# Optimization experiments

Hardware: AMD Instinct MI355X
Metric: run time of the kernel (lower is better)

The kernel has to match this reference:

```python
import jax, jax.numpy as jnp
import numpy as np

N_LEVELS = 16
F_PER_LEVEL = 2
LOG2_T = 19
TABLE_SIZE = 1 << LOG2_T
BASE_RES = 16.0
FINEST_RES = 512.0
# W == H == 512 -> x1 = y1 = 1.0
BOX_MIN = jnp.array([-1.0, -1.0], dtype=jnp.float32)
BOX_MAX = jnp.array([1.0, 1.0], dtype=jnp.float32)
# corner offsets, same order as torch BOX_OFFSETS: (0,0),(0,1),(1,0),(1,1)
OFFSETS = jnp.array([[i, j] for i in (0, 1) for j in (0, 1)], dtype=jnp.int32)
PRIME0 = jnp.uint32(1)
PRIME1 = jnp.uint32(2654435761)
HASH_MASK = jnp.uint32(TABLE_SIZE - 1)


def setup_inputs() -> dict:
    key = jax.random.key(0)
    ks = jax.random.split(key, 8)
    B, P = 4, 262144
    coord_2D = jax.random.uniform(ks[0], (B, P, 2), dtype=jnp.float32)  # in [0,1) subset of box
    embeddings = jax.random.normal(ks[1], (N_LEVELS, TABLE_SIZE, F_PER_LEVEL), dtype=jnp.float32)
    d_in = 2 + N_LEVELS * F_PER_LEVEL  # 34
    W0 = jax.random.normal(ks[2], (d_in, 256), dtype=jnp.float32) * 0.05
    b0 = jnp.zeros((256,), dtype=jnp.float32)
    W1 = jax.random.normal(ks[3], (256, 256), dtype=jnp.float32) * 0.05
    b1 = jnp.zeros((256,), dtype=jnp.float32)
    W2 = jax.random.normal(ks[4], (256, 3), dtype=jnp.float32) * 0.05
    b2 = jnp.zeros((3,), dtype=jnp.float32)
    return {"coord_2D": coord_2D, "embeddings": embeddings,
            "W0": W0, "b0": b0, "W1": W1, "b1": b1, "W2": W2, "b2": b2}


def _hash(corners_int32):
    # corners: [N,4,2] int32; xor of per-dim prime products, masked to table size (uint32 wraparound semantics)
    c = corners_int32.astype(jnp.uint32)
    h = (c[..., 0] * PRIME0) ^ (c[..., 1] * PRIME1)
    return (h & HASH_MASK).astype(jnp.int32)


def _encode(xy, embeddings):
    # xy: [N,2]; embeddings: [L, T, F]
    b = np.exp((np.log(FINEST_RES) - np.log(BASE_RES)) / (N_LEVELS - 1))
    resolutions = jnp.floor(BASE_RES * (b ** jnp.arange(N_LEVELS, dtype=jnp.float32)))  # [L]

    def level_encode(table, res):
        grid = (BOX_MAX - BOX_MIN) / res                     # [2]
        bl = jnp.floor((xy - BOX_MIN) / grid).astype(jnp.int32)  # bottom-left cell idx [N,2]
        vmin = bl.astype(xy.dtype) * grid + BOX_MIN          # voxel min vertex [N,2]
        w = (xy - vmin) / grid                               # bilinear weights [N,2]
        corners = bl[:, None, :] + OFFSETS                   # [N,4,2]
        emb = table[_hash(corners)]                          # gather: [N,4,F]
        wx = w[:, 0:1]
        wy = w[:, 1:2]
        c00 = emb[:, 0] * (1 - wx) + emb[:, 2] * wx
        c01 = emb[:, 1] * (1 - wx) + emb[:, 3] * wx
        return c00 * (1 - wy) + c01 * wy                     # [N,F]

    enc = jax.vmap(level_encode)(embeddings, resolutions)    # [L,N,F]
    return jnp.moveaxis(enc, 0, 1).reshape(xy.shape[0], N_LEVELS * F_PER_LEVEL)


def reference(coord_2D, embeddings, W0, b0, W1, b1, W2, b2):
    B = coord_2D.shape[0]
    xy = jnp.clip(coord_2D.reshape(-1, 2), BOX_MIN, BOX_MAX)
    enc = _encode(xy, embeddings)
    points_enc = jnp.concatenate([xy, enc], axis=-1)         # [N, 34]
    feat = jax.nn.relu(points_enc @ W0 + b0)
    feat = jax.nn.relu(feat @ W1 + b1)
    rgb = jax.nn.sigmoid(feat @ W2 + b2)
    return rgb.reshape(B, -1, 3)
```

## Files before the change

kernel.cpp:

```cpp
#include <hip/hip_runtime.h>
#include <hip/hip_bf16.h>
#include <cstdint>
#include <cstddef>

#define N_LEVELS   16
#define LOG2_T     19
#define TABLE_SIZE (1u << LOG2_T)
#define HASH_MASK  (TABLE_SIZE - 1u)
#define PRIME1     2654435761u

#define TPB 256
#define BT  64

typedef __attribute__((ext_vector_type(8))) short short8;
typedef __attribute__((ext_vector_type(4))) float floatx4;
typedef __attribute__((ext_vector_type(2))) float f32x2;

__device__ __forceinline__ constexpr float resf(int l) {
    constexpr float r[N_LEVELS] = {
        16.f, 20.f, 25.f, 32.f, 40.f, 50.f, 64.f, 80.f,
        101.f, 128.f, 161.f, 203.f, 256.f, 322.f, 406.f, 512.f
    };
    return r[l];
}

__device__ __forceinline__ unsigned short f2bf(float x) {
    union { float f; uint32_t u; } v; v.f = x;
    const uint32_t u = v.u;
    return (unsigned short)((u + 0x7fffu + ((u >> 16) & 1u)) >> 16);
}

__device__ __forceinline__ uint32_t pk_bf16(float a, float b) {
#if __has_builtin(__builtin_amdgcn_cvt_pk_bf16_f32)
    typedef __attribute__((ext_vector_type(2))) __bf16 bf16x2;
    bf16x2 v = __builtin_amdgcn_cvt_pk_bf16_f32(a, b);
    uint32_t u; __builtin_memcpy(&u, &v, 4); return u;
#else
    return (uint32_t)f2bf(a) | ((uint32_t)f2bf(b) << 16);
#endif
}

__device__ __forceinline__ int fswz(int row, int cb) {
    return (row << 7) + (cb ^ ((row & 7) << 4));
}
__device__ __forceinline__ int hswz(int row, int cb) {
    const int c = row & 7;
    return (row << 9) + (cb ^ ((c << 4) ^ (c << 6)));
}

__global__ void pack_weights(const float* __restrict__ W0,
                             const float* __restrict__ W1,
                             const float* __restrict__ W2,
                             unsigned short* __restrict__ ws)
{
    const int f = blockIdx.x;
    const int lane = threadIdx.x;
    const int q = lane >> 4, r = lane & 15;
    int layer, kt, nt;
    if (f < 32)       { layer = 0; kt = f >> 4;        nt = f & 15; }
    else if (f < 160) { layer = 1; kt = (f - 32) >> 4; nt = (f - 32) & 15; }
    else              { layer = 2; kt = f - 160;       nt = 0; }
    unsigned short vals[8];
    #pragma unroll
    for (int j = 0; j < 8; ++j) {
        const int k = kt * 32 + q * 8 + j;
        const int n = nt * 16 + r;
        float v = 0.f;
        if (layer == 0) {
            if (k < 32)       v = W0[(2 + k) * 256 + n];
            else if (k == 32) v = W0[0 * 256 + n];
            else if (k == 33) v = W0[1 * 256 + n];
        } else if (layer == 1) {
            v = W1[k * 256 + n];
        } else {
            if (n < 3) v = W2[k * 3 + n];
        }
        vals[j] = f2bf(v);
    }
    uint4 pk;
    pk.x = (uint32_t)vals[0] | ((uint32_t)vals[1] << 16);
    pk.y = (uint32_t)vals[2] | ((uint32_t)vals[3] << 16);
    pk.z = (uint32_t)vals[4] | ((uint32_t)vals[5] << 16);
    pk.w = (uint32_t)vals[6] | ((uint32_t)vals[7] << 16);
    *(uint4*)(ws + (size_t)f * 1024 + lane * 8) = pk;
}

template<int G>
__device__ __forceinline__ uint4 encode4(float x, float y, const char* __restrict__ ebase)
{
    uint32_t vv[4];
    #pragma unroll
    for (int i = 0; i < 4; ++i) {
        const int l = 4 * G + i;
        const float res  = resf(l);
        const float grid = 2.0f / res;
        const float invg = res * 0.5f;
        const float tx = (x + 1.0f) / grid;
        const float ty = (y + 1.0f) / grid;
        const int bx = (int)floorf(tx);
        const int by = (int)floorf(ty);
        const float wx = (x - ((float)bx * grid - 1.0f)) * invg;
        const float wy = (y - ((float)by * grid - 1.0f)) * invg;
        const uint32_t hy0 = (uint32_t)by * PRIME1;
        const uint32_t hy1 = hy0 + PRIME1;
        const uint32_t ux0 = (uint32_t)bx;
        const uint32_t ux1 = ux0 + 1u;
        const uint32_t lb = (uint32_t)l << (LOG2_T + 3);
        const f32x2 e00 = *(const f32x2*)(ebase + (lb + (((ux0 ^ hy0) & HASH_MASK) << 3)));
        const f32x2 e01 = *(const f32x2*)(ebase + (lb + (((ux0 ^ hy1) & HASH_MASK) << 3)));
        const f32x2 e10 = *(const f32x2*)(ebase + (lb + (((ux1 ^ hy0) & HASH_MASK) << 3)));
        const f32x2 e11 = *(const f32x2*)(ebase + (lb + (((ux1 ^ hy1) & HASH_MASK) << 3)));
        const float owx = 1.f - wx, owy = 1.f - wy;
        const float f0 = (e00.x * owx + e10.x * wx) * owy + (e01.x * owx + e11.x * wx) * wy;
        const float f1 = (e00.y * owx + e10.y * wx) * owy + (e01.y * owx + e11.y * wx) * wy;
        vv[i] = pk_bf16(f0, f1);
    }
    uint4 v; v.x = vv[0]; v.y = vv[1]; v.z = vv[2]; v.w = vv[3];
    return v;
}

__device__ __forceinline__ uint2 bias_relu_pk(const floatx4 a, const float4 bias)
{
    const f32x2 z = {0.f, 0.f};
    f32x2 v01 = {a[0], a[1]};
    f32x2 v23 = {a[2], a[3]};
    const f32x2 b01 = {bias.x, bias.y};
    const f32x2 b23 = {bias.z, bias.w};
    v01 += b01;
    v23 += b23;
    v01 = __builtin_elementwise_max(v01, z);
    v23 = __builtin_elementwise_max(v23, z);
    uint2 r;
    r.x = pk_bf16(v01.x, v01.y);
    r.y = pk_bf16(v23.x, v23.y);
    return r;
}

__global__ __launch_bounds__(TPB, 4)
void fused_ngp_mlp(const float2* __restrict__ xy,
                   const float* __restrict__ emb,
                   const unsigned short* __restrict__ wpack,
                   const float* __restrict__ b0,
                   const float* __restrict__ b1,
                   const float* __restrict__ b2,
                   float* __restrict__ out, int npoints)
{
    __shared__ __attribute__((aligned(16))) unsigned char feat[BT * 128];
    __shared__ __attribute__((aligned(16))) unsigned char h[BT * 512];

    const int t = threadIdx.x;
    const int p0 = blockIdx.x * BT;
    const int wave = t >> 6;
    const int lane = t & 63;
    const int q = lane >> 4, r = lane & 15;

    {
        const int p = t >> 2;
        const int sg = t & 3;
        const int gp = p0 + p;
        float x = 0.f, y = 0.f;
        if (gp < npoints) {
            const float2 c = xy[gp];
            x = fminf(fmaxf(c.x, -1.f), 1.f);
            y = fminf(fmaxf(c.y, -1.f), 1.f);
        }
        uint4 z = {0u, 0u, 0u, 0u};
        if (sg == 0) z.x = pk_bf16(x, y);
        *(uint4*)(feat + fswz(p, 64 + 16 * sg)) = z;
    }

    {
        const int p = lane;
        const int gp = p0 + p;
        float x = 0.f, y = 0.f;
        if (gp < npoints) {
            const float2 c = xy[gp];
            x = fminf(fmaxf(c.x, -1.f), 1.f);
            y = fminf(fmaxf(c.y, -1.f), 1.f);
        }
        const char* ebase = (const char*)emb;
        uint4 v;
        switch (wave) {
            case 0:  v = encode4<0>(x, y, ebase); break;
            case 1:  v = encode4<1>(x, y, ebase); break;
            case 2:  v = encode4<2>(x, y, ebase); break;
            default: v = encode4<3>(x, y, ebase); break;
        }
        *(uint4*)(feat + fswz(p, 16 * wave)) = v;
    }
    __syncthreads();

    const unsigned short* w0p = wpack;
    const unsigned short* w1p = wpack + 32 * 1024;
    const unsigned short* w2p = wpack + 160 * 1024;

    {
        floatx4 acc[4][4];
        #pragma unroll
        for (int mti = 0; mti < 4; ++mti)
            #pragma unroll
            for (int nt = 0; nt < 4; ++nt)
                acc[mti][nt] = floatx4{0.f, 0.f, 0.f, 0.f};
        #pragma unroll
        for (int kt = 0; kt < 2; ++kt) {
            short8 a[4], b[4];
            #pragma unroll
            for (int mti = 0; mti < 4; ++mti)
                a[mti] = *(const short8*)(w0p + (size_t)(kt * 16 + wave * 4 + mti) * 1024 + lane * 8);
            #pragma unroll
            for (int nt = 0; nt < 4; ++nt)
                b[nt] = *(const short8*)(feat + fswz(16 * nt + r, 64 * kt + 16 * q));
            #pragma unroll
            for (int mti = 0; mti < 4; ++mti)
                #pragma unroll
                for (int nt = 0; nt < 4; ++nt)
                    acc[mti][nt] = __builtin_amdgcn_mfma_f32_16x16x32_bf16(a[mti], b[nt], acc[mti][nt], 0, 0, 0);
        }
        #pragma unroll
        for (int mti = 0; mti < 4; ++mti) {
            const int col = (wave * 4 + mti) * 16 + 4 * q;
            const float4 bias = *(const float4*)&b0[col];
            #pragma unroll
            for (int nt = 0; nt < 4; ++nt) {
                const uint2 v = bias_relu_pk(acc[mti][nt], bias);
                *(uint2*)(h + hswz(16 * nt + r, 2 * col)) = v;
            }
        }
    }
    __syncthreads();

    {
        floatx4 acc[4][4];
        #pragma unroll
        for (int mti = 0; mti < 4; ++mti)
            #pragma unroll
            for (int nt = 0; nt < 4; ++nt)
                acc[mti][nt] = floatx4{0.f, 0.f, 0.f, 0.f};
        #pragma unroll 2
        for (int kt = 0; kt < 8; ++kt) {
            short8 a[4], b[4];
            #pragma unroll
            for (int mti = 0; mti < 4; ++mti)
                a[mti] = *(const short8*)(w1p + (size_t)(kt * 16 + wave * 4 + mti) * 1024 + lane * 8);
            #pragma unroll
            for (int nt = 0; nt < 4; ++nt)
                b[nt] = *(const short8*)(h + hswz(16 * nt + r, 64 * kt + 16 * q));
            #pragma unroll
            for (int mti = 0; mti < 4; ++mti)
                #pragma unroll
                for (int nt = 0; nt < 4; ++nt)
                    acc[mti][nt] = __builtin_amdgcn_mfma_f32_16x16x32_bf16(a[mti], b[nt], acc[mti][nt], 0, 0, 0);
        }
        __syncthreads();
        #pragma unroll
        for (int mti = 0; mti < 4; ++mti) {
            const int col = (wave * 4 + mti) * 16 + 4 * q;
            const float4 bias = *(const float4*)&b1[col];
            #pragma unroll
            for (int nt = 0; nt < 4; ++nt) {
                const uint2 v = bias_relu_pk(acc[mti][nt], bias);
                *(uint2*)(h + hswz(16 * nt + r, 2 * col)) = v;
            }
        }
    }
    __syncthreads();

    {
        floatx4 acc = floatx4{0.f, 0.f, 0.f, 0.f};
        #pragma unroll
        for (int kt = 0; kt < 8; ++kt) {
            const short8 a = *(const short8*)(w2p + (size_t)kt * 1024 + lane * 8);
            const short8 b = *(const short8*)(h + hswz(16 * wave + r, 64 * kt + 16 * q));
            acc = __builtin_amdgcn_mfma_f32_16x16x32_bf16(a, b, acc, 0, 0, 0);
        }
        if (q == 0) {
            const int gp = p0 + 16 * wave + r;
            if (gp < npoints) {
                #pragma unroll
                for (int reg = 0; reg < 3; ++reg) {
                    const float s = acc[reg] + b2[reg];
                    out[(size_t)gp * 3 + reg] = 1.f / (1.f + expf(-s));
                }
            }
        }
    }
}

extern "C" void kernel_launch(void* const* d_in, const int* in_sizes, int n_in,
                              void* d_out, int out_size, void* d_ws, size_t ws_size,
                              hipStream_t stream) {
    const float* coord = (const float*)d_in[0];
    const float* emb   = (const float*)d_in[1];
    const float* W0    = (const float*)d_in[2];
    const float* b0    = (const float*)d_in[3];
    const float* W1    = (const float*)d_in[4];
    const float* b1    = (const float*)d_in[5];
    const float* W2    = (const float*)d_in[6];
    const float* b2    = (const float*)d_in[7];
    float* out = (float*)d_out;
    unsigned short* ws = (unsigned short*)d_ws;

    const int npoints = in_sizes[0] / 2;
    const int blocks  = (npoints + BT - 1) / BT;

    hipLaunchKernelGGL(pack_weights, dim3(168), dim3(64), 0, stream, W0, W1, W2, ws);
    hipLaunchKernelGGL(fused_ngp_mlp, dim3(blocks), dim3(TPB), 0, stream,
                       (const float2*)coord, emb, ws, b0, b1, b2, out, npoints);
}
```

Measured before the change: 355.1 us.

## Use 512-thread blocks: 8 waves split hash levels and MLP N tiles

Doubles the block to 8 waves. Each wave now encodes 2 hash levels instead of 4, and the MLP tiles are split so each wave computes 4 M tiles by 2 point tiles. The separate feat LDS buffer is aliased onto h, with an extra barrier before layer-0 results overwrite it, which cuts LDS per block. The aim is more waves in flight to hide gather latency and lower per-thread register pressure, at the cost of loading each weight fragment from global twice per block and adding synchronisation.

```diff
diff --git a/kernel.cpp b/kernel.cpp
--- a/kernel.cpp
+++ b/kernel.cpp
@@ -9,7 +9,7 @@
 #define HASH_MASK  (TABLE_SIZE - 1u)
 #define PRIME1     2654435761u
 
-#define TPB 256
+#define TPB 512
 #define BT  64
 
 typedef __attribute__((ext_vector_type(8))) short short8;
@@ -85,13 +85,13 @@
     *(uint4*)(ws + (size_t)f * 1024 + lane * 8) = pk;
 }
 
-template<int G>
-__device__ __forceinline__ uint4 encode4(float x, float y, const char* __restrict__ ebase)
+template<int W>
+__device__ __forceinline__ uint2 encode2(float x, float y, const char* __restrict__ ebase)
 {
-    uint32_t vv[4];
+    uint32_t vv[2];
     #pragma unroll
-    for (int i = 0; i < 4; ++i) {
-        const int l = 4 * G + i;
+    for (int i = 0; i < 2; ++i) {
+        const int l = 2 * W + i;
         const float res  = resf(l);
         const float grid = 2.0f / res;
         const float invg = res * 0.5f;
@@ -115,7 +115,7 @@
         const float f1 = (e00.y * owx + e10.y * wx) * owy + (e01.y * owx + e11.y * wx) * wy;
         vv[i] = pk_bf16(f0, f1);
     }
-    uint4 v; v.x = vv[0]; v.y = vv[1]; v.z = vv[2]; v.w = vv[3];
+    uint2 v; v.x = vv[0]; v.y = vv[1];
     return v;
 }
 
@@ -136,7 +136,7 @@
     return r;
 }
 
-__global__ __launch_bounds__(TPB, 4)
+__global__ __launch_bounds__(TPB, 6)
 void fused_ngp_mlp(const float2* __restrict__ xy,
                    const float* __restrict__ emb,
                    const unsigned short* __restrict__ wpack,
@@ -145,48 +145,55 @@
                    const float* __restrict__ b2,
                    float* __restrict__ out, int npoints)
 {
-    __shared__ __attribute__((aligned(16))) unsigned char feat[BT * 128];
     __shared__ __attribute__((aligned(16))) unsigned char h[BT * 512];
+    unsigned char* feat = h;
 
     const int t = threadIdx.x;
     const int p0 = blockIdx.x * BT;
     const int wave = t >> 6;
     const int lane = t & 63;
     const int q = lane >> 4, r = lane & 15;
+    const int wn = wave & 3;
+    const int wp = wave >> 2;
 
     {
-        const int p = t >> 2;
-        const int sg = t & 3;
-        const int gp = p0 + p;
+        const int p = t >> 3;
+        const int sg = t & 7;
+        uint2 z = {0u, 0u};
+        if (sg == 0) {
+            const int gp = p0 + p;
+            float x = 0.f, y = 0.f;
+            if (gp < npoints) {
+                const float2 c = xy[gp];
+                x = fminf(fmaxf(c.x, -1.f), 1.f);
+                y = fminf(fmaxf(c.y, -1.f), 1.f);
+            }
+            z.x = pk_bf16(x, y);
+        }
+        *(uint2*)(feat + fswz(p, 64 + 8 * sg)) = z;
+    }
+
+    {
+        const int gp = p0 + lane;
         float x = 0.f, y = 0.f;
         if (gp < npoints) {
             const float2 c = xy[gp];
             x = fminf(fmaxf(c.x, -1.f), 1.f);
             y = fminf(fmaxf(c.y, -1.f), 1.f);
         }
-        uint4 z = {0u, 0u, 0u, 0u};
-        if (sg == 0) z.x = pk_bf16(x, y);
-        *(uint4*)(feat + fswz(p, 64 + 16 * sg)) = z;
-    }
-
-    {
-        const int p = lane;
-        const int gp = p0 + p;
-        float x = 0.f, y = 0.f;
-        if (gp < npoints) {
-            const float2 c = xy[gp];
-            x = fminf(fmaxf(c.x, -1.f), 1.f);
-            y = fminf(fmaxf(c.y, -1.f), 1.f);
-        }
         const char* ebase = (const char*)emb;
-        uint4 v;
+        uint2 v;
         switch (wave) {
-            case 0:  v = encode4<0>(x, y, ebase); break;
-            case 1:  v = encode4<1>(x, y, ebase); break;
-            case 2:  v = encode4<2>(x, y, ebase); break;
-            default: v = encode4<3>(x, y, ebase); break;
-        }
-        *(uint4*)(feat + fswz(p, 16 * wave)) = v;
+            case 0:  v = encode2<0>(x, y, ebase); break;
+            case 1:  v = encode2<1>(x, y, ebase); break;
+            case 2:  v = encode2<2>(x, y, ebase); break;
+            case 3:  v = encode2<3>(x, y, ebase); break;
+            case 4:  v = encode2<4>(x, y, ebase); break;
+            case 5:  v = encode2<5>(x, y, ebase); break;
+            case 6:  v = encode2<6>(x, y, ebase); break;
+            default: v = encode2<7>(x, y, ebase); break;
+        }
+        *(uint2*)(feat + fswz(lane, 8 * wave)) = v;
     }
     __syncthreads();
 
@@ -195,77 +202,76 @@
     const unsigned short* w2p = wpack + 160 * 1024;
 
     {
-        floatx4 acc[4][4];
+        floatx4 acc[4][2];
         #pragma unroll
         for (int mti = 0; mti < 4; ++mti)
             #pragma unroll
-            for (int nt = 0; nt < 4; ++nt)
+            for (int nt = 0; nt < 2; ++nt)
                 acc[mti][nt] = floatx4{0.f, 0.f, 0.f, 0.f};
         #pragma unroll
         for (int kt = 0; kt < 2; ++kt) {
-            short8 a[4], b[4];
-            #pragma unroll
-            for (int mti = 0; mti < 4; ++mti)
-                a[mti] = *(const short8*)(w0p + (size_t)(kt * 16 + wave * 4 + mti) * 1024 + lane * 8);
-            #pragma unroll
-            for (int nt = 0; nt < 4; ++nt)
-                b[nt] = *(const short8*)(feat + fswz(16 * nt + r, 64 * kt + 16 * q));
-            #pragma unroll
-            for (int mti = 0; mti < 4; ++mti)
+            short8 b[2];
+            #pragma unroll
+            for (int nt = 0; nt < 2; ++nt)
+                b[nt] = *(const short8*)(feat + fswz((wp * 2 + nt) * 16 + r, 64 * kt + 16 * q));
+            #pragma unroll
+            for (int mti = 0; mti < 4; ++mti) {
+                const short8 a = *(const short8*)(w0p + (size_t)(kt * 16 + wn * 4 + mti) * 1024 + lane * 8);
                 #pragma unroll
-                for (int nt = 0; nt < 4; ++nt)
-                    acc[mti][nt] = __builtin_amdgcn_mfma_f32_16x16x32_bf16(a[mti], b[nt], acc[mti][nt], 0, 0, 0);
-        }
+                for (int nt = 0; nt < 2; ++nt)
+                    acc[mti][nt] = __builtin_amdgcn_mfma_f32_16x16x32_bf16(a, b[nt], acc[mti][nt], 0, 0, 0);
+            }
+        }
+        __syncthreads();
         #pragma unroll
         for (int mti = 0; mti < 4; ++mti) {
-            const int col = (wave * 4 + mti) * 16 + 4 * q;
+            const int col = (wn * 4 + mti) * 16 + 4 * q;
             const float4 bias = *(const float4*)&b0[col];
             #pragma unroll
-            for (int nt = 0; nt < 4; ++nt) {
+            for (int nt = 0; nt < 2; ++nt) {
                 const uint2 v = bias_relu_pk(acc[mti][nt], bias);
-                *(uint2*)(h + hswz(16 * nt + r, 2 * col)) = v;
+                *(uint2*)(h + hswz((wp * 2 + nt) * 16 + r, 2 * col)) = v;
             }
         }
     }
     __syncthreads();
 
     {
-        floatx4 acc[4][4];
+        floatx4 acc[4][2];
         #pragma unroll
         for (int mti = 0; mti < 4; ++mti)
             #pragma unroll
-            for (int nt = 0; nt < 4; ++nt)
+            for (int nt = 0; nt < 2; ++nt)
                 acc[mti][nt] = floatx4{0.f, 0.f, 0.f, 0.f};
         #pragma unroll 2
         for (int kt = 0; kt < 8; ++kt) {
-            short8 a[4], b[4];
-            #pragma unroll
-            for (int mti = 0; mti < 4; ++mti)
-                a[mti] = *(const short8*)(w1p + (size_t)(kt * 16 + wave * 4 + mti) * 1024 + lane * 8);
-            #pragma unroll
-            for (int nt = 0; nt < 4; ++nt)
-                b[nt] = *(const short8*)(h + hswz(16 * nt + r, 64 * kt + 16 * q));
-            #pragma unroll
-            for (int mti = 0; mti < 4; ++mti)
+            short8 b[2];
+            #pragma unroll
+            for (int nt = 0; nt < 2; ++nt)
+                b[nt] = *(const short8*)(h + hswz((wp * 2 + nt) * 16 + r, 64 * kt + 16 * q));
+            #pragma unroll
+            for (int mti = 0; mti < 4; ++mti) {
+                const short8 a = *(const short8*)(w1p + (size_t)(kt * 16 + wn * 4 + mti) * 1024 + lane * 8);
                 #pragma unroll
-                for (int nt = 0; nt < 4; ++nt)
-                    acc[mti][nt] = __builtin_amdgcn_mfma_f32_16x16x32_bf16(a[mti], b[nt], acc[mti][nt], 0, 0, 0);
+                for (int nt = 0; nt < 2; ++nt)
+                    acc[mti][nt] = __builtin_amdgcn_mfma_f32_16x16x32_bf16(a, b[nt], acc[mti][nt], 0, 0, 0);
+            }
         }
         __syncthreads();
         #pragma unroll
         for (int mti = 0; mti < 4; ++mti) {
-            const int col = (wave * 4 + mti) * 16 + 4 * q;
+            const int col = (wn * 4 + mti) * 16 + 4 * q;
             const float4 bias = *(const float4*)&b1[col];
             #pragma unroll
-            for (int nt = 0; nt < 4; ++nt) {
+            for (int nt = 0; nt < 2; ++nt) {
                 const uint2 v = bias_relu_pk(acc[mti][nt], bias);
-                *(uint2*)(h + hswz(16 * nt + r, 2 * col)) = v;
+                *(uint2*)(h + hswz((wp * 2 + nt) * 16 + r, 2 * col)) = v;
             }
         }
     }
     __syncthreads();
 
-    {
+    if (wave < 4) {
         floatx4 acc = floatx4{0.f, 0.f, 0.f, 0.f};
         #pragma unroll
         for (int kt = 0; kt < 8; ++kt) {
```

New measurement: 428.8 us. 1.21x slower.

## Fold xy rows of W0 into epilogue FMAs and alias feature LDS into hidden buffer

Applied to the files above, without the earlier changes.

The xy contribution to layer 0 is now computed in fp32 with scalar FMAs in the bias/ReLU epilogue, using W0 rows read directly from global memory. This halves the first MFMA K-loop to one 32-wide step over the hash features only. The separate feature shared buffer is removed by aliasing it onto the hidden buffer, with an added barrier before overwriting. The aim is fewer MFMAs and less LDS per block, which may raise occupancy. The cost is extra coordinate loads per thread and more per-element FMAs, and it relies on pack_weights laying out the K rows so that tile 0 holds only the encoding features.

```diff
diff --git a/kernel.cpp b/kernel.cpp
--- a/kernel.cpp
+++ b/kernel.cpp
@@ -140,13 +140,14 @@
 void fused_ngp_mlp(const float2* __restrict__ xy,
                    const float* __restrict__ emb,
                    const unsigned short* __restrict__ wpack,
+                   const float* __restrict__ W0g,
                    const float* __restrict__ b0,
                    const float* __restrict__ b1,
                    const float* __restrict__ b2,
                    float* __restrict__ out, int npoints)
 {
-    __shared__ __attribute__((aligned(16))) unsigned char feat[BT * 128];
     __shared__ __attribute__((aligned(16))) unsigned char h[BT * 512];
+    unsigned char* feat = h;
 
     const int t = threadIdx.x;
     const int p0 = blockIdx.x * BT;
@@ -154,19 +155,15 @@
     const int lane = t & 63;
     const int q = lane >> 4, r = lane & 15;
 
-    {
-        const int p = t >> 2;
-        const int sg = t & 3;
-        const int gp = p0 + p;
-        float x = 0.f, y = 0.f;
-        if (gp < npoints) {
-            const float2 c = xy[gp];
-            x = fminf(fmaxf(c.x, -1.f), 1.f);
-            y = fminf(fmaxf(c.y, -1.f), 1.f);
-        }
-        uint4 z = {0u, 0u, 0u, 0u};
-        if (sg == 0) z.x = pk_bf16(x, y);
-        *(uint4*)(feat + fswz(p, 64 + 16 * sg)) = z;
+    float cx[4], cy[4];
+    #pragma unroll
+    for (int nt = 0; nt < 4; ++nt) {
+        const int gp2 = p0 + 16 * nt + r;
+        float2 c;
+        if (gp2 < npoints) c = xy[gp2];
+        else { c.x = 0.f; c.y = 0.f; }
+        cx[nt] = fminf(fmaxf(c.x, -1.f), 1.f);
+        cy[nt] = fminf(fmaxf(c.y, -1.f), 1.f);
     }
 
     {
@@ -201,28 +198,38 @@
             #pragma unroll
             for (int nt = 0; nt < 4; ++nt)
                 acc[mti][nt] = floatx4{0.f, 0.f, 0.f, 0.f};
-        #pragma unroll
-        for (int kt = 0; kt < 2; ++kt) {
+        {
             short8 a[4], b[4];
             #pragma unroll
             for (int mti = 0; mti < 4; ++mti)
-                a[mti] = *(const short8*)(w0p + (size_t)(kt * 16 + wave * 4 + mti) * 1024 + lane * 8);
+                a[mti] = *(const short8*)(w0p + (size_t)(wave * 4 + mti) * 1024 + lane * 8);
             #pragma unroll
             for (int nt = 0; nt < 4; ++nt)
-                b[nt] = *(const short8*)(feat + fswz(16 * nt + r, 64 * kt + 16 * q));
+                b[nt] = *(const short8*)(feat + fswz(16 * nt + r, 16 * q));
             #pragma unroll
             for (int mti = 0; mti < 4; ++mti)
                 #pragma unroll
                 for (int nt = 0; nt < 4; ++nt)
                     acc[mti][nt] = __builtin_amdgcn_mfma_f32_16x16x32_bf16(a[mti], b[nt], acc[mti][nt], 0, 0, 0);
         }
+        __syncthreads();
         #pragma unroll
         for (int mti = 0; mti < 4; ++mti) {
             const int col = (wave * 4 + mti) * 16 + 4 * q;
             const float4 bias = *(const float4*)&b0[col];
+            const float4 w0x  = *(const float4*)&W0g[col];
+            const float4 w0y  = *(const float4*)&W0g[256 + col];
             #pragma unroll
             for (int nt = 0; nt < 4; ++nt) {
-                const uint2 v = bias_relu_pk(acc[mti][nt], bias);
+                const float x = cx[nt], y = cy[nt];
+                floatx4 aa = acc[mti][nt];
+                aa[0] += bias.x + x * w0x.x + y * w0y.x;
+                aa[1] += bias.y + x * w0x.y + y * w0y.y;
+                aa[2] += bias.z + x * w0x.z + y * w0y.z;
+                aa[3] += bias.w + x * w0x.w + y * w0y.w;
+                uint2 v;
+                v.x = pk_bf16(fmaxf(aa[0], 0.f), fmaxf(aa[1], 0.f));
+                v.y = pk_bf16(fmaxf(aa[2], 0.f), fmaxf(aa[3], 0.f));
                 *(uint2*)(h + hswz(16 * nt + r, 2 * col)) = v;
             }
         }
@@ -305,5 +312,5 @@
 
     hipLaunchKernelGGL(pack_weights, dim3(168), dim3(64), 0, stream, W0, W1, W2, ws);
     hipLaunchKernelGGL(fused_ngp_mlp, dim3(blocks), dim3(TPB), 0, stream,
-                       (const float2*)coord, emb, ws, b0, b1, b2, out, npoints);
-}
+                       (const float2*)coord, emb, ws, W0, b0, b1, b2, out, npoints);
+}
```

Result: slower. 385.0 us (+8.4%).

## Precompute dense per-level grid tables from hash table for contiguous corner loads

Applied to the files above, without the earlier changes.

Adds a pre-pass that expands each level's hashed embedding lookups into a dense row-major grid of corner values, sized to the level resolution plus one. The encoder then fetches two adjacent corners with one 16-byte load per row instead of four scattered hash gathers, which cuts random-access traffic and hashing arithmetic. The feature staging buffer now aliases the hidden buffer, with an extra barrier before the overwrite, to free shared memory. It costs an extra kernel launch and about 5.7 MB of workspace, and falls back to the hash path if the workspace is too small.

```diff
diff --git a/kernel.cpp b/kernel.cpp
--- a/kernel.cpp
+++ b/kernel.cpp
@@ -12,9 +12,13 @@
 #define TPB 256
 #define BT  64
 
+#define W_BYTES    344064
+#define DENSE_TOT  716544
+
 typedef __attribute__((ext_vector_type(8))) short short8;
 typedef __attribute__((ext_vector_type(4))) float floatx4;
 typedef __attribute__((ext_vector_type(2))) float f32x2;
+typedef float f32x4u __attribute__((ext_vector_type(4), aligned(8)));
 
 __device__ __forceinline__ constexpr float resf(int l) {
     constexpr float r[N_LEVELS] = {
@@ -22,6 +26,15 @@
         101.f, 128.f, 161.f, 203.f, 256.f, 322.f, 406.f, 512.f
     };
     return r[l];
+}
+__device__ __forceinline__ constexpr int dimf(int l) {
+    constexpr int d[N_LEVELS] = {18,22,27,34,42,52,66,82,103,130,163,205,258,324,408,514};
+    return d[l];
+}
+__device__ __forceinline__ constexpr int offf(int l) {
+    constexpr int o[N_LEVELS] = {0,324,808,1537,2693,4457,7161,11517,
+                                 18241,28850,45750,72319,114344,180908,285884,452348};
+    return o[l];
 }
 
 __device__ __forceinline__ unsigned short f2bf(float x) {
@@ -46,6 +59,27 @@
 __device__ __forceinline__ int hswz(int row, int cb) {
     const int c = row & 7;
     return (row << 9) + (cb ^ ((c << 4) ^ (c << 6)));
+}
+
+__global__ void k_dense(const float* __restrict__ emb, f32x2* __restrict__ dense, int total)
+{
+    const int i = blockIdx.x * 256 + threadIdx.x;
+    if (i >= total) return;
+    const f32x2* e2 = (const f32x2*)emb;
+#define DL(L, NEXT)                                                          \
+    if (i < (NEXT)) {                                                        \
+        const int local = i - offf(L);                                       \
+        const int uy = local / dimf(L);                                      \
+        const int ux = local - uy * dimf(L);                                 \
+        const uint32_t h = ((uint32_t)ux ^ ((uint32_t)uy * PRIME1)) & HASH_MASK; \
+        dense[i] = e2[(size_t)(L) * TABLE_SIZE + h];                         \
+        return;                                                              \
+    }
+    DL(0,  324)     DL(1,  808)     DL(2,  1537)    DL(3,  2693)
+    DL(4,  4457)    DL(5,  7161)    DL(6,  11517)   DL(7,  18241)
+    DL(8,  28850)   DL(9,  45750)   DL(10, 72319)   DL(11, 114344)
+    DL(12, 180908)  DL(13, 285884)  DL(14, 452348)  DL(15, 716544)
+#undef DL
 }
 
 __global__ void pack_weights(const float* __restrict__ W0,
@@ -86,7 +120,35 @@
 }
 
 template<int G>
-__device__ __forceinline__ uint4 encode4(float x, float y, const char* __restrict__ ebase)
+__device__ __forceinline__ uint4 encode4d(float x, float y, const f32x2* __restrict__ dense)
+{
+    uint32_t vv[4];
+    #pragma unroll
+    for (int i = 0; i < 4; ++i) {
+        const int l = 4 * G + i;
+        const float res  = resf(l);
+        const float grid = 2.0f / res;
+        const float invg = res * 0.5f;
+        const float tx = (x + 1.0f) / grid;
+        const float ty = (y + 1.0f) / grid;
+        const int bx = (int)floorf(tx);
+        const int by = (int)floorf(ty);
+        const float wx = (x - ((float)bx * grid - 1.0f)) * invg;
+        const float wy = (y - ((float)by * grid - 1.0f)) * invg;
+        const int base = offf(l) + by * dimf(l) + bx;
+        const f32x4u r0 = *(const f32x4u*)(dense + base);
+        const f32x4u r1 = *(const f32x4u*)(dense + base + dimf(l));
+        const float owx = 1.f - wx, owy = 1.f - wy;
+        const float f0 = (r0.x * owx + r0.z * wx) * owy + (r1.x * owx + r1.z * wx) * wy;
+        const float f1 = (r0.y * owx + r0.w * wx) * owy + (r1.y * owx + r1.w * wx) * wy;
+        vv[i] = pk_bf16(f0, f1);
+    }
+    uint4 v; v.x = vv[0]; v.y = vv[1]; v.z = vv[2]; v.w = vv[3];
+    return v;
+}
+
+template<int G>
+__device__ __forceinline__ uint4 encode4h(float x, float y, const char* __restrict__ ebase)
 {
     uint32_t vv[4];
     #pragma unroll
@@ -136,17 +198,19 @@
     return r;
 }
 
+template<bool DENSE>
 __global__ __launch_bounds__(TPB, 4)
 void fused_ngp_mlp(const float2* __restrict__ xy,
                    const float* __restrict__ emb,
+                   const f32x2* __restrict__ dense,
                    const unsigned short* __restrict__ wpack,
                    const float* __restrict__ b0,
                    const float* __restrict__ b1,
                    const float* __restrict__ b2,
                    float* __restrict__ out, int npoints)
 {
-    __shared__ __attribute__((aligned(16))) unsigned char feat[BT * 128];
     __shared__ __attribute__((aligned(16))) unsigned char h[BT * 512];
+    unsigned char* feat = h;
 
     const int t = threadIdx.x;
     const int p0 = blockIdx.x * BT;
@@ -178,13 +242,22 @@
             x = fminf(fmaxf(c.x, -1.f), 1.f);
             y = fminf(fmaxf(c.y, -1.f), 1.f);
         }
-        const char* ebase = (const char*)emb;
         uint4 v;
-        switch (wave) {
-            case 0:  v = encode4<0>(x, y, ebase); break;
-            case 1:  v = encode4<1>(x, y, ebase); break;
-            case 2:  v = encode4<2>(x, y, ebase); break;
-            default: v = encode4<3>(x, y, ebase); break;
+        if (DENSE) {
+            switch (wave) {
+                case 0:  v = encode4d<0>(x, y, dense); break;
+                case 1:  v = encode4d<1>(x, y, dense); break;
+                case 2:  v = encode4d<2>(x, y, dense); break;
+                default: v = encode4d<3>(x, y, dense); break;
+            }
+        } else {
+            const char* ebase = (const char*)emb;
+            switch (wave) {
+                case 0:  v = encode4h<0>(x, y, ebase); break;
+                case 1:  v = encode4h<1>(x, y, ebase); break;
+                case 2:  v = encode4h<2>(x, y, ebase); break;
+                default: v = encode4h<3>(x, y, ebase); break;
+            }
         }
         *(uint4*)(feat + fswz(p, 16 * wave)) = v;
     }
@@ -216,6 +289,7 @@
                 for (int nt = 0; nt < 4; ++nt)
                     acc[mti][nt] = __builtin_amdgcn_mfma_f32_16x16x32_bf16(a[mti], b[nt], acc[mti][nt], 0, 0, 0);
         }
+        __syncthreads();
         #pragma unroll
         for (int mti = 0; mti < 4; ++mti) {
             const int col = (wave * 4 + mti) * 16 + 4 * q;
@@ -298,12 +372,23 @@
     const float* W2    = (const float*)d_in[6];
     const float* b2    = (const float*)d_in[7];
     float* out = (float*)d_out;
-    unsigned short* ws = (unsigned short*)d_ws;
+    unsigned char* ws = (unsigned char*)d_ws;
 
     const int npoints = in_sizes[0] / 2;
     const int blocks  = (npoints + BT - 1) / BT;
 
-    hipLaunchKernelGGL(pack_weights, dim3(168), dim3(64), 0, stream, W0, W1, W2, ws);
-    hipLaunchKernelGGL(fused_ngp_mlp, dim3(blocks), dim3(TPB), 0, stream,
-                       (const float2*)coord, emb, ws, b0, b1, b2, out, npoints);
-}
+    unsigned short* wp = (unsigned short*)ws;
+    hipLaunchKernelGGL(pack_weights, dim3(168), dim3(64), 0, stream, W0, W1, W2, wp);
+
+    const size_t required = (size_t)W_BYTES + (size_t)DENSE_TOT * 8;
+    if (ws_size >= required) {
+        f32x2* dense = (f32x2*)(ws + W_BYTES);
+        hipLaunchKernelGGL(k_dense, dim3((DENSE_TOT + 255) / 256), dim3(256), 0, stream,
+                           emb, dense, DENSE_TOT);
+        hipLaunchKernelGGL((fused_ngp_mlp<true>), dim3(blocks), dim3(TPB), 0, stream,
+                           (const float2*)coord, emb, dense, wp, b0, b1, b2, out, npoints);
+    } else {
+        hipLaunchKernelGGL((fused_ngp_mlp<false>), dim3(blocks), dim3(TPB), 0, stream,
+                           (const float2*)coord, emb, (const f32x2*)nullptr, wp, b0, b1, b2, out, npoints);
+    }
+}
```

Result: no change. 358.6 us (+1.0%).
